# Kernel optimization log

Measured on AMD Instinct MI355X. Metric: run time of the kernel, lower is better.

Reference implementation:

```python
import jax, jax.numpy as jnp
import numpy as np

T, D, O, L, R = 8192, 4096, 4096, 8, 16  # tokens, in_dim, out_dim, max_loras, lora_rank


def setup_inputs() -> dict:
    key = jax.random.key(0)
    k0, k1, k2, k3, k4 = jax.random.split(key, 5)
    x = jax.random.normal(k0, (T, D), dtype=jnp.float32)
    weight = jax.random.normal(k1, (O, D), dtype=jnp.float32) * 0.02   # base Linear weight
    lora_a = jax.random.normal(k2, (L, R, D), dtype=jnp.float32) * 0.02  # stacked A (slice dim squeezed)
    lora_b = jax.random.normal(k3, (L, O, R), dtype=jnp.float32) * 0.02  # stacked B
    token_lora_idx = jax.random.randint(k4, (T,), 0, L, dtype=jnp.int32)  # per-token adapter id
    return {"x": x, "weight": weight, "lora_a": lora_a, "lora_b": lora_b,
            "token_lora_idx": token_lora_idx}


def reference(x, weight, lora_a, lora_b, token_lora_idx):
    # base linear (no bias)
    base = jnp.einsum('td,od->to', x, weight)
    # punica add_lora_linear, single slice, scale = 1.0:
    # per-token gather of A/B expressed as a one-hot contraction (small L, rank R)
    onehot = jax.nn.one_hot(token_lora_idx, lora_a.shape[0], dtype=x.dtype)  # [T, L]
    shrink = jnp.einsum('td,lrd->tlr', x, lora_a)          # [T, L, R] (tiny: R=16)
    s = jnp.einsum('tlr,tl->tr', shrink, onehot)           # select this token's adapter
    delta = jnp.einsum('tr,lor,tl->to', s, lora_b, onehot) # expand + scatter-add
    return base + delta
```

## Files before the change

### kernel.cpp

```cpp
#include <hip/hip_runtime.h>
#include <hip/hip_bf16.h>
#include <stdint.h>

#define T_TOK 8192
#define DIM 4096
#define ODIM 4096
#define NL 8
#define RANK 16
#define KAUG 4224

__device__ __forceinline__ uint16_t f2b(float x) {
    uint32_t u = __builtin_bit_cast(uint32_t, x);
    u += 0x7fffu + ((u >> 16) & 1u);
    return (uint16_t)(u >> 16);
}

typedef __attribute__((ext_vector_type(4))) float floatx4;
typedef __attribute__((ext_vector_type(8))) __bf16 bf16x8;

__device__ __forceinline__ void load_lds16(const uint16_t* g, uint16_t* l) {
    __builtin_amdgcn_global_load_lds(
        (const __attribute__((address_space(1))) uint32_t*)g,
        (__attribute__((address_space(3))) uint32_t*)l, 16, 0, 0);
}

__global__ __launch_bounds__(256) void pack_all(const float* __restrict__ x,
                                                const float* __restrict__ W,
                                                const float* __restrict__ la,
                                                const float* __restrict__ lb,
                                                uint16_t* __restrict__ xaug,
                                                uint16_t* __restrict__ waug,
                                                uint16_t* __restrict__ aall) {
    int b = blockIdx.x;
    int tid = threadIdx.x;
    const float* src;
    uint16_t* dst;
    if (b < ODIM)               { src = W  + (size_t)b * DIM;                 dst = waug + (size_t)b * KAUG; }
    else if (b < ODIM + T_TOK)  { int t = b - ODIM;
                                  src = x  + (size_t)t * DIM;                 dst = xaug + (size_t)t * KAUG; }
    else                        { int r = b - ODIM - T_TOK;
                                  src = la + (size_t)r * DIM;                 dst = aall + (size_t)r * DIM; }
#pragma unroll
    for (int k = 0; k < 4; ++k) {
        int i4 = k * 256 + tid;
        float4 v = ((const float4*)src)[i4];
        ushort4 bv;
        bv.x = f2b(v.x); bv.y = f2b(v.y); bv.z = f2b(v.z); bv.w = f2b(v.w);
        *(ushort4*)(dst + (size_t)i4 * 4) = bv;
    }
    if (b < ODIM && tid < NL * RANK) {
        int l = tid >> 4, r = tid & 15;
        dst[DIM + tid] = f2b(lb[((size_t)l * ODIM + b) * RANK + r]);
    }
}

#define SBM 32
__global__ __launch_bounds__(256) void shrink_gemm(const uint16_t* __restrict__ xa,
                                                   const uint16_t* __restrict__ aall,
                                                   const int* __restrict__ idx,
                                                   uint16_t* __restrict__ xaug) {
    __shared__ uint16_t sA[SBM * 64];
    __shared__ uint16_t sB[128 * 64];
    int tid = threadIdx.x, lane = tid & 63, wid = tid >> 6;
    int bm = blockIdx.x;
    int q = lane >> 4, r16 = lane & 15;

    int rS = tid >> 3;
    int kcS = (tid & 7) ^ (rS & 7);
    const uint16_t* gA = xa + (size_t)(bm * SBM + rS) * KAUG + kcS * 8;
    const uint16_t* gB0 = aall + (size_t)(rS) * DIM + kcS * 8;
    const uint16_t* gB1 = aall + (size_t)(32 + rS) * DIM + kcS * 8;
    const uint16_t* gB2 = aall + (size_t)(64 + rS) * DIM + kcS * 8;
    const uint16_t* gB3 = aall + (size_t)(96 + rS) * DIM + kcS * 8;
    uint16_t* lA  = sA + wid * 512;
    uint16_t* lB0 = sB + wid * 512;
    uint16_t* lB1 = sB + 2048 + wid * 512;
    uint16_t* lB2 = sB + 4096 + wid * 512;
    uint16_t* lB3 = sB + 6144 + wid * 512;

    int sw0 = (q ^ (r16 & 7)) * 8;
    int sw1 = ((4 + q) ^ (r16 & 7)) * 8;

    floatx4 acc[2][2];
#pragma unroll
    for (int i = 0; i < 2; ++i)
#pragma unroll
        for (int j = 0; j < 2; ++j) acc[i][j] = (floatx4){0.f, 0.f, 0.f, 0.f};

    for (int k0 = 0; k0 < DIM; k0 += 64) {
        __syncthreads();
        load_lds16(gA + k0, lA);
        load_lds16(gB0 + k0, lB0);
        load_lds16(gB1 + k0, lB1);
        load_lds16(gB2 + k0, lB2);
        load_lds16(gB3 + k0, lB3);
        __syncthreads();
#pragma unroll
        for (int kk = 0; kk < 2; ++kk) {
            int sw = kk ? sw1 : sw0;
            bf16x8 af[2], bv[2];
#pragma unroll
            for (int i = 0; i < 2; ++i)
                af[i] = *(const bf16x8*)(sA + (i * 16 + r16) * 64 + sw);
#pragma unroll
            for (int j = 0; j < 2; ++j)
                bv[j] = *(const bf16x8*)(sB + (wid * 32 + j * 16 + r16) * 64 + sw);
#pragma unroll
            for (int i = 0; i < 2; ++i)
#pragma unroll
                for (int j = 0; j < 2; ++j)
                    acc[i][j] = __builtin_amdgcn_mfma_f32_16x16x32_bf16(af[i], bv[j], acc[i][j], 0, 0, 0);
        }
    }
#pragma unroll
    for (int i = 0; i < 2; ++i) {
#pragma unroll
        for (int j = 0; j < 2; ++j) {
            int p = wid * 32 + j * 16 + r16;
            int lp = p >> 4;
#pragma unroll
            for (int e = 0; e < 4; ++e) {
                int t = bm * SBM + i * 16 + q * 4 + e;
                uint16_t v = (idx[t] == lp) ? f2b(acc[i][j][e]) : (uint16_t)0;
                xaug[(size_t)t * KAUG + DIM + p] = v;
            }
        }
    }
}

#define BM 128
#define BN 128

__global__ __launch_bounds__(256) void gemm_aug(const uint16_t* __restrict__ A,
                                                const uint16_t* __restrict__ B,
                                                float* __restrict__ C) {
    __shared__ uint16_t sA[BM * 64];
    __shared__ uint16_t sB[BN * 64];

    int tid = threadIdx.x, lane = tid & 63, wid = tid >> 6;
    int bn = blockIdx.x, bm = blockIdx.y;
    int wm = (wid & 1) * 64, wn = (wid >> 1) * 64;
    int q = lane >> 4, r16 = lane & 15;

    int rS = tid >> 3;
    int kcS = (tid & 7) ^ (rS & 7);
    const uint16_t* gA[4];
    const uint16_t* gB[4];
    uint16_t* lA[4];
    uint16_t* lB[4];
#pragma unroll
    for (int c = 0; c < 4; ++c) {
        gA[c] = A + (size_t)(bm * BM + c * 32 + rS) * KAUG + kcS * 8;
        gB[c] = B + (size_t)(bn * BN + c * 32 + rS) * KAUG + kcS * 8;
        lA[c] = sA + c * 2048 + wid * 512;
        lB[c] = sB + c * 2048 + wid * 512;
    }

    int sw0 = (q ^ (r16 & 7)) * 8;
    int sw1 = ((4 + q) ^ (r16 & 7)) * 8;

    floatx4 acc[4][4];
#pragma unroll
    for (int i = 0; i < 4; ++i)
#pragma unroll
        for (int j = 0; j < 4; ++j) acc[i][j] = (floatx4){0.f, 0.f, 0.f, 0.f};

    for (int k0 = 0; k0 < KAUG; k0 += 64) {
        __syncthreads();
#pragma unroll
        for (int c = 0; c < 4; ++c) {
            load_lds16(gA[c] + k0, lA[c]);
            load_lds16(gB[c] + k0, lB[c]);
        }
        __syncthreads();
#pragma unroll
        for (int kk = 0; kk < 2; ++kk) {
            int sw = kk ? sw1 : sw0;
            bf16x8 af[4], bv[4];
#pragma unroll
            for (int i = 0; i < 4; ++i)
                af[i] = *(const bf16x8*)(sA + (wm + i * 16 + r16) * 64 + sw);
#pragma unroll
            for (int j = 0; j < 4; ++j)
                bv[j] = *(const bf16x8*)(sB + (wn + j * 16 + r16) * 64 + sw);
#pragma unroll
            for (int i = 0; i < 4; ++i)
#pragma unroll
                for (int j = 0; j < 4; ++j)
                    acc[i][j] = __builtin_amdgcn_mfma_f32_16x16x32_bf16(af[i], bv[j], acc[i][j], 0, 0, 0);
        }
    }

#pragma unroll
    for (int i = 0; i < 4; ++i) {
#pragma unroll
        for (int j = 0; j < 4; ++j) {
            int col = bn * BN + wn + j * 16 + r16;
#pragma unroll
            for (int e = 0; e < 4; ++e) {
                int row = bm * BM + wm + i * 16 + q * 4 + e;
                C[(size_t)row * ODIM + col] = acc[i][j][e];
            }
        }
    }
}

extern "C" void kernel_launch(void* const* d_in, const int* in_sizes, int n_in,
                              void* d_out, int out_size, void* d_ws, size_t ws_size,
                              hipStream_t stream) {
    const float* x  = (const float*)d_in[0];
    const float* W  = (const float*)d_in[1];
    const float* la = (const float*)d_in[2];
    const float* lb = (const float*)d_in[3];
    const int* idx  = (const int*)d_in[4];
    float* out = (float*)d_out;

    uint16_t* xaug = (uint16_t*)d_ws;
    uint16_t* waug = xaug + (size_t)T_TOK * KAUG;
    uint16_t* aall = waug + (size_t)ODIM * KAUG;

    hipLaunchKernelGGL(pack_all, dim3(ODIM + T_TOK + NL * RANK), dim3(256), 0, stream,
                       x, W, la, lb, xaug, waug, aall);
    hipLaunchKernelGGL(shrink_gemm, dim3(T_TOK / SBM), dim3(256), 0, stream,
                       xaug, aall, idx, xaug);
    hipLaunchKernelGGL(gemm_aug, dim3(ODIM / BN, T_TOK / BM), dim3(256), 0, stream,
                       xaug, waug, out);
}
```

Before: 611.7 us.

## Fuse x bf16 packing into shrink GEMM, swizzle GEMM tile order, use nontemporal stores

Converting x to bf16 now happens inside the shrink kernel. It converts fp32 x tiles, writes them to xaug with nontemporal stores, and feeds the same tiles straight from LDS into the shrink MFMA. This removes the separate pass that re-read bf16 x from global memory. The main GEMM uses a 1D grid remapped into panels of 8 M-tiles to improve L2 reuse, and writes its output with nontemporal stores. The shrink kernel now uses a smaller M tile (16) and a deeper K step (128), which changes occupancy and the cost of reloading the LoRA A matrix per block.

```diff
diff --git a/kernel.cpp b/kernel.cpp
--- a/kernel.cpp
+++ b/kernel.cpp
@@ -23,107 +23,114 @@
         (const __attribute__((address_space(1))) uint32_t*)g,
         (__attribute__((address_space(3))) uint32_t*)l, 16, 0, 0);
 }
-
-__global__ __launch_bounds__(256) void pack_all(const float* __restrict__ x,
-                                                const float* __restrict__ W,
-                                                const float* __restrict__ la,
-                                                const float* __restrict__ lb,
-                                                uint16_t* __restrict__ xaug,
-                                                uint16_t* __restrict__ waug,
-                                                uint16_t* __restrict__ aall) {
+__device__ __forceinline__ void nt_store_u4(uint16_t* p, ushort4 v) {
+    __builtin_nontemporal_store(__builtin_bit_cast(unsigned long long, v),
+                                (unsigned long long*)p);
+}
+
+__global__ __launch_bounds__(256) void pack_w(const float* __restrict__ W,
+                                              const float* __restrict__ la,
+                                              const float* __restrict__ lb,
+                                              uint16_t* __restrict__ waug,
+                                              uint16_t* __restrict__ aall) {
     int b = blockIdx.x;
     int tid = threadIdx.x;
-    const float* src;
-    uint16_t* dst;
-    if (b < ODIM)               { src = W  + (size_t)b * DIM;                 dst = waug + (size_t)b * KAUG; }
-    else if (b < ODIM + T_TOK)  { int t = b - ODIM;
-                                  src = x  + (size_t)t * DIM;                 dst = xaug + (size_t)t * KAUG; }
-    else                        { int r = b - ODIM - T_TOK;
-                                  src = la + (size_t)r * DIM;                 dst = aall + (size_t)r * DIM; }
-#pragma unroll
-    for (int k = 0; k < 4; ++k) {
-        int i4 = k * 256 + tid;
-        float4 v = ((const float4*)src)[i4];
-        ushort4 bv;
-        bv.x = f2b(v.x); bv.y = f2b(v.y); bv.z = f2b(v.z); bv.w = f2b(v.w);
-        *(ushort4*)(dst + (size_t)i4 * 4) = bv;
-    }
-    if (b < ODIM && tid < NL * RANK) {
-        int l = tid >> 4, r = tid & 15;
-        dst[DIM + tid] = f2b(lb[((size_t)l * ODIM + b) * RANK + r]);
-    }
-}
-
-#define SBM 32
-__global__ __launch_bounds__(256) void shrink_gemm(const uint16_t* __restrict__ xa,
+    if (b < ODIM) {
+        const float4* src = (const float4*)(W + (size_t)b * DIM);
+        uint16_t* dst = waug + (size_t)b * KAUG;
+#pragma unroll
+        for (int k = 0; k < 4; ++k) {
+            int i4 = k * 256 + tid;
+            float4 v = src[i4];
+            ushort4 bv;
+            bv.x = f2b(v.x); bv.y = f2b(v.y); bv.z = f2b(v.z); bv.w = f2b(v.w);
+            nt_store_u4(dst + (size_t)i4 * 4, bv);
+        }
+        if (tid < NL * RANK) {
+            int l = tid >> 4, r = tid & 15;
+            dst[DIM + tid] = f2b(lb[((size_t)l * ODIM + b) * RANK + r]);
+        }
+    } else {
+        int rr = b - ODIM;
+        const float4* src = (const float4*)(la + (size_t)rr * DIM);
+        uint16_t* dst = aall + (size_t)rr * DIM;
+#pragma unroll
+        for (int k = 0; k < 4; ++k) {
+            int i4 = k * 256 + tid;
+            float4 v = src[i4];
+            ushort4 bv;
+            bv.x = f2b(v.x); bv.y = f2b(v.y); bv.z = f2b(v.z); bv.w = f2b(v.w);
+            *(ushort4*)(dst + (size_t)i4 * 4) = bv;
+        }
+    }
+}
+
+#define SBM 16
+__global__ __launch_bounds__(256) void shrink_pack(const float* __restrict__ x,
                                                    const uint16_t* __restrict__ aall,
                                                    const int* __restrict__ idx,
                                                    uint16_t* __restrict__ xaug) {
-    __shared__ uint16_t sA[SBM * 64];
-    __shared__ uint16_t sB[128 * 64];
+    __shared__ uint16_t sA[SBM * 128];
+    __shared__ uint16_t sB[128 * 128];
     int tid = threadIdx.x, lane = tid & 63, wid = tid >> 6;
-    int bm = blockIdx.x;
+    int t0 = blockIdx.x * SBM;
     int q = lane >> 4, r16 = lane & 15;
 
-    int rS = tid >> 3;
-    int kcS = (tid & 7) ^ (rS & 7);
-    const uint16_t* gA = xa + (size_t)(bm * SBM + rS) * KAUG + kcS * 8;
-    const uint16_t* gB0 = aall + (size_t)(rS) * DIM + kcS * 8;
-    const uint16_t* gB1 = aall + (size_t)(32 + rS) * DIM + kcS * 8;
-    const uint16_t* gB2 = aall + (size_t)(64 + rS) * DIM + kcS * 8;
-    const uint16_t* gB3 = aall + (size_t)(96 + rS) * DIM + kcS * 8;
-    uint16_t* lA  = sA + wid * 512;
-    uint16_t* lB0 = sB + wid * 512;
-    uint16_t* lB1 = sB + 2048 + wid * 512;
-    uint16_t* lB2 = sB + 4096 + wid * 512;
-    uint16_t* lB3 = sB + 6144 + wid * 512;
-
-    int sw0 = (q ^ (r16 & 7)) * 8;
-    int sw1 = ((4 + q) ^ (r16 & 7)) * 8;
-
-    floatx4 acc[2][2];
-#pragma unroll
-    for (int i = 0; i < 2; ++i)
-#pragma unroll
-        for (int j = 0; j < 2; ++j) acc[i][j] = (floatx4){0.f, 0.f, 0.f, 0.f};
-
-    for (int k0 = 0; k0 < DIM; k0 += 64) {
-        __syncthreads();
-        load_lds16(gA + k0, lA);
-        load_lds16(gB0 + k0, lB0);
-        load_lds16(gB1 + k0, lB1);
-        load_lds16(gB2 + k0, lB2);
-        load_lds16(gB3 + k0, lB3);
-        __syncthreads();
-#pragma unroll
-        for (int kk = 0; kk < 2; ++kk) {
-            int sw = kk ? sw1 : sw0;
-            bf16x8 af[2], bv[2];
-#pragma unroll
-            for (int i = 0; i < 2; ++i)
-                af[i] = *(const bf16x8*)(sA + (i * 16 + r16) * 64 + sw);
-#pragma unroll
-            for (int j = 0; j < 2; ++j)
-                bv[j] = *(const bf16x8*)(sB + (wid * 32 + j * 16 + r16) * 64 + sw);
-#pragma unroll
-            for (int i = 0; i < 2; ++i)
-#pragma unroll
-                for (int j = 0; j < 2; ++j)
-                    acc[i][j] = __builtin_amdgcn_mfma_f32_16x16x32_bf16(af[i], bv[j], acc[i][j], 0, 0, 0);
-        }
-    }
-#pragma unroll
-    for (int i = 0; i < 2; ++i) {
-#pragma unroll
-        for (int j = 0; j < 2; ++j) {
-            int p = wid * 32 + j * 16 + r16;
-            int lp = p >> 4;
-#pragma unroll
-            for (int e = 0; e < 4; ++e) {
-                int t = bm * SBM + i * 16 + q * 4 + e;
-                uint16_t v = (idx[t] == lp) ? f2b(acc[i][j][e]) : (uint16_t)0;
-                xaug[(size_t)t * KAUG + DIM + p] = v;
+    int rSB = tid >> 4;
+    int kcB = (tid & 15) ^ (rSB & 15);
+    const uint16_t* gB[8];
+    uint16_t* lB[8];
+#pragma unroll
+    for (int c = 0; c < 8; ++c) {
+        gB[c] = aall + (size_t)(c * 16 + rSB) * DIM + kcB * 8;
+        lB[c] = sB + c * 2048 + wid * 512;
+    }
+
+    floatx4 acc[2];
+    acc[0] = (floatx4){0.f, 0.f, 0.f, 0.f};
+    acc[1] = (floatx4){0.f, 0.f, 0.f, 0.f};
+
+    for (int k0 = 0; k0 < DIM; k0 += 128) {
+        __syncthreads();
+#pragma unroll
+        for (int c = 0; c < 8; ++c) load_lds16(gB[c] + k0, lB[c]);
+#pragma unroll
+        for (int p = 0; p < 2; ++p) {
+            int u = p * 256 + tid;
+            int row = u >> 5;
+            int c4 = u & 31;
+            float4 v = *(const float4*)(x + (size_t)(t0 + row) * DIM + k0 + c4 * 4);
+            ushort4 bv;
+            bv.x = f2b(v.x); bv.y = f2b(v.y); bv.z = f2b(v.z); bv.w = f2b(v.w);
+            nt_store_u4(xaug + (size_t)(t0 + row) * KAUG + k0 + c4 * 4, bv);
+            int chunk = c4 >> 1, half = c4 & 1;
+            int slot = chunk ^ (row & 15);
+            *(ushort4*)(sA + row * 128 + slot * 8 + half * 4) = bv;
+        }
+        __syncthreads();
+#pragma unroll
+        for (int kk = 0; kk < 4; ++kk) {
+            int ca = (4 * kk + q) ^ r16;
+            bf16x8 af = *(const bf16x8*)(sA + r16 * 128 + ca * 8);
+#pragma unroll
+            for (int j = 0; j < 2; ++j) {
+                bf16x8 bv = *(const bf16x8*)(sB + (wid * 32 + j * 16 + r16) * 128 + ca * 8);
+                acc[j] = __builtin_amdgcn_mfma_f32_16x16x32_bf16(af, bv, acc[j], 0, 0, 0);
             }
+        }
+    }
+    int idxv[4];
+#pragma unroll
+    for (int e = 0; e < 4; ++e) idxv[e] = idx[t0 + q * 4 + e];
+#pragma unroll
+    for (int j = 0; j < 2; ++j) {
+        int p = wid * 32 + j * 16 + r16;
+        int lp = p >> 4;
+#pragma unroll
+        for (int e = 0; e < 4; ++e) {
+            int t = t0 + q * 4 + e;
+            uint16_t v = (idxv[e] == lp) ? f2b(acc[j][e]) : (uint16_t)0;
+            xaug[(size_t)t * KAUG + DIM + p] = v;
         }
     }
 }
@@ -138,7 +145,11 @@
     __shared__ uint16_t sB[BN * 64];
 
     int tid = threadIdx.x, lane = tid & 63, wid = tid >> 6;
-    int bn = blockIdx.x, bm = blockIdx.y;
+    int lid = blockIdx.x;
+    int panel = lid >> 8;
+    int rem = lid & 255;
+    int bn = rem >> 3;
+    int bm = (panel << 3) | (rem & 7);
     int wm = (wid & 1) * 64, wn = (wid >> 1) * 64;
     int q = lane >> 4, r16 = lane & 15;
 
@@ -199,7 +210,7 @@
 #pragma unroll
             for (int e = 0; e < 4; ++e) {
                 int row = bm * BM + wm + i * 16 + q * 4 + e;
-                C[(size_t)row * ODIM + col] = acc[i][j][e];
+                __builtin_nontemporal_store(acc[i][j][e], &C[(size_t)row * ODIM + col]);
             }
         }
     }
@@ -219,10 +230,10 @@
     uint16_t* waug = xaug + (size_t)T_TOK * KAUG;
     uint16_t* aall = waug + (size_t)ODIM * KAUG;
 
-    hipLaunchKernelGGL(pack_all, dim3(ODIM + T_TOK + NL * RANK), dim3(256), 0, stream,
-                       x, W, la, lb, xaug, waug, aall);
-    hipLaunchKernelGGL(shrink_gemm, dim3(T_TOK / SBM), dim3(256), 0, stream,
-                       xaug, aall, idx, xaug);
-    hipLaunchKernelGGL(gemm_aug, dim3(ODIM / BN, T_TOK / BM), dim3(256), 0, stream,
+    hipLaunchKernelGGL(pack_w, dim3(ODIM + NL * RANK), dim3(256), 0, stream,
+                       W, la, lb, waug, aall);
+    hipLaunchKernelGGL(shrink_pack, dim3(T_TOK / SBM), dim3(256), 0, stream,
+                       x, aall, idx, xaug);
+    hipLaunchKernelGGL(gemm_aug, dim3((T_TOK / BM) * (ODIM / BN)), dim3(256), 0, stream,
                        xaug, waug, out);
 }
```

Result: slower. 657.5 us (+7.5%).
